# Kernel tuning notes

Hardware: AMD Instinct MI355X
Metric: run time of the kernel (lower is better)

The kernel has to match this reference:

```python
import jax, jax.numpy as jnp
import numpy as np

NO_EDGE_OFFSET_T_NORM = 2.0    # pushes no_edge above data range so min() ignores it
NO_EDGE_OFFSET_T_CONORM = -1.0 # pushes no_edge below data range so max() ignores it


def _daa_layer(x, sel, is_t_norm):
    """One DAALayer with a single operator for all nodes (LAYER_WISE init).

    x:   [B, in_features] float
    sel: [out_features, in_features] int, edge type per (node, input):
         0 = no_edge (value 0 + operator-dependent offset), 1 = normal_edge (value x)
    """
    off = NO_EDGE_OFFSET_T_NORM if is_t_norm else NO_EDGE_OFFSET_T_CONORM
    # [B, out, in]: gather edge values per node according to hard routing
    vals = jnp.where(sel[None, :, :] == 1, x[:, None, :], jnp.float32(off))
    # t-norm 'min' / t-conorm 'max' reduction over incoming edges
    return vals.min(axis=-1) if is_t_norm else vals.max(axis=-1)


def setup_inputs() -> dict:
    key = jax.random.key(0)
    k1, k2, k3 = jax.random.split(key, 3)
    B, IN, HID = 256, 1024, 512
    x = jax.random.uniform(k1, (B, IN), dtype=jnp.float32)
    # hard gumbel-softmax over all-ones logits == uniform edge-type choice
    sel0 = jax.random.randint(k2, (HID, IN), 0, 2)  # layer 0: 1024 -> 512
    sel1 = jax.random.randint(k3, (IN, HID), 0, 2)  # layer 1: 512 -> 1024
    return {"x": x, "sel0": sel0, "sel1": sel1}


def reference(x, sel0, sel1):
    h = _daa_layer(x, sel0, True)    # layer 0: T_Norm.min on all nodes
    out = _daa_layer(h, sel1, False)  # layer 1: T_Conorm.max on all nodes
    return out
```

## Files before the change

kernel.cpp:

```cpp
#include <hip/hip_runtime.h>
#include <hip/hip_fp16.h>


#define H_PINF 0x7C00u
#define H_NINF 0xFC00u

__device__ __forceinline__ unsigned pk_add(unsigned a, unsigned b) {
    unsigned r; asm("v_pk_add_f16 %0, %1, %2" : "=v"(r) : "v"(a), "v"(b)); return r;
}
__device__ __forceinline__ unsigned pk_min(unsigned a, unsigned b) {
    unsigned r; asm("v_pk_min_f16 %0, %1, %2" : "=v"(r) : "v"(a), "v"(b)); return r;
}
__device__ __forceinline__ unsigned pk_max(unsigned a, unsigned b) {
    unsigned r; asm("v_pk_max_f16 %0, %1, %2" : "=v"(r) : "v"(a), "v"(b)); return r;
}
__device__ __forceinline__ unsigned hpk(float a, float b) {
    return (unsigned)__half_as_ushort(__float2half(a))
         | ((unsigned)__half_as_ushort(__float2half(b)) << 16);
}
__device__ __forceinline__ float h2f(unsigned short u) {
    __half h = *reinterpret_cast<__half*>(&u);
    return __half2float(h);
}
__device__ __forceinline__ unsigned selpk(int a, int b, unsigned inf) {
    return (a ? 0u : inf) | ((b ? 0u : inf) << 16);
}

__global__ __launch_bounds__(1024) void daa_l0(
    const float* __restrict__ x, const int* __restrict__ sel0,
    uint4* __restrict__ hS)
{
    __shared__ unsigned aW[8 * 512];
    __shared__ uint4 xL[2][16 * 65];
    __shared__ unsigned red32[16 * 4 * 64];
    __shared__ unsigned mrg32[4 * 64];

    const int tid  = threadIdx.x;
    const int lane = tid & 63;
    const int s    = __builtin_amdgcn_readfirstlane(tid >> 6);
    const int bch  = blockIdx.x & 3;
    const int j    = blockIdx.x >> 2;
    const int b0   = bch * 64;

    {
        const int4* sp = (const int4*)sel0;
        const int row = tid >> 7, ch = tid & 127;
        const int4 v0 = sp[(size_t)(8 * j + row) * 256 + ch * 2 + 0];
        const int4 v1 = sp[(size_t)(8 * j + row) * 256 + ch * 2 + 1];
        unsigned* dst = &aW[row * 512 + ch * 4];
        dst[0] = selpk(v0.x, v0.y, H_PINF);
        dst[1] = selpk(v0.z, v0.w, H_PINF);
        dst[2] = selpk(v1.x, v1.y, H_PINF);
        dst[3] = selpk(v1.z, v1.w, H_PINF);
    }

    const int br = tid >> 4, cg = tid & 15;
#define STAGE(T, BUF)                                                      \
    do {                                                                   \
        const float* xr = x + (size_t)(b0 + br) * 1024 + (T) * 128 + cg * 8; \
        const float4 f0 = ((const float4*)xr)[0];                          \
        const float4 f1 = ((const float4*)xr)[1];                          \
        uint4 w;                                                           \
        w.x = hpk(f0.x, f0.y);  w.y = hpk(f0.z, f0.w);                     \
        w.z = hpk(f1.x, f1.y);  w.w = hpk(f1.z, f1.w);                     \
        xL[BUF][cg * 65 + br] = w;                                         \
    } while (0)

    STAGE(0, 0);
    __syncthreads();

    unsigned acc[8];
#pragma unroll
    for (int r = 0; r < 8; ++r) acc[r] = hpk(2.0f, 2.0f);

#pragma unroll
    for (int t = 0; t < 8; ++t) {
        if (t + 1 < 8) STAGE(t + 1, (t + 1) & 1);
        const uint4 xv = xL[t & 1][s * 65 + lane];
#pragma unroll
        for (int r = 0; r < 8; ++r) {
            const unsigned* a = &aW[r * 512 + t * 64 + s * 4];
            acc[r] = pk_min(acc[r], pk_add(xv.x, a[0]));
            acc[r] = pk_min(acc[r], pk_add(xv.y, a[1]));
            acc[r] = pk_min(acc[r], pk_add(xv.z, a[2]));
            acc[r] = pk_min(acc[r], pk_add(xv.w, a[3]));
        }
        __syncthreads();
    }
#undef STAGE

    {
#pragma unroll
        for (int u = 0; u < 4; ++u) {
            const unsigned flo = pk_min(acc[2 * u + 0], acc[2 * u + 0] >> 16);
            const unsigned fhi = pk_min(acc[2 * u + 1], acc[2 * u + 1] >> 16);
            red32[(s * 4 + u) * 64 + lane] = (flo & 0xffffu) | (fhi << 16);
        }
    }
    __syncthreads();

    if (tid < 256) {
        const int u = tid >> 6, ln = tid & 63;
        unsigned m = red32[u * 64 + ln];
#pragma unroll
        for (int ss = 1; ss < 16; ++ss)
            m = pk_min(m, red32[(ss * 4 + u) * 64 + ln]);
        mrg32[u * 64 + ln] = m;
    }
    __syncthreads();

    if (tid < 64) {
        uint4 w;
        w.x = mrg32[0 * 64 + tid];
        w.y = mrg32[1 * 64 + tid];
        w.z = mrg32[2 * 64 + tid];
        w.w = mrg32[3 * 64 + tid];
        hS[(size_t)bch * 4096 + (size_t)j * 64 + tid] = w;
    }
}

__global__ __launch_bounds__(1024) void daa_l1(
    const uint4* __restrict__ hS, const int* __restrict__ sel1,
    float* __restrict__ out)
{
    __shared__ unsigned aW[16 * 256];
    __shared__ unsigned red32[16 * 8 * 64];
    __shared__ float redf[16 * 65];

    const int tid  = threadIdx.x;
    const int lane = tid & 63;
    const int s    = __builtin_amdgcn_readfirstlane(tid >> 6);
    const int bch  = blockIdx.x & 3;
    const int j2   = blockIdx.x >> 2;
    const int b0   = bch * 64;

    {
        const int4* sp = (const int4*)sel1;
        const int row = tid >> 6, ch = tid & 63;
        const int4 v0 = sp[(size_t)(16 * j2 + row) * 128 + ch * 2 + 0];
        const int4 v1 = sp[(size_t)(16 * j2 + row) * 128 + ch * 2 + 1];
        unsigned* dst = &aW[row * 256 + ch * 4];
        dst[0] = selpk(v0.x, v0.y, H_NINF);
        dst[1] = selpk(v0.z, v0.w, H_NINF);
        dst[2] = selpk(v1.x, v1.y, H_NINF);
        dst[3] = selpk(v1.z, v1.w, H_NINF);
    }

    uint4 xh[4];
#pragma unroll
    for (int k = 0; k < 4; ++k)
        xh[k] = hS[(size_t)bch * 4096 + (size_t)(s * 4 + k) * 64 + lane];

    __syncthreads();

    unsigned acc[16];
#pragma unroll
    for (int r = 0; r < 16; ++r) acc[r] = hpk(-1.0f, -1.0f);

#pragma unroll
    for (int r = 0; r < 16; ++r) {
        const unsigned* a = &aW[r * 256 + s * 16];
#pragma unroll
        for (int k = 0; k < 4; ++k) {
            acc[r] = pk_max(acc[r], pk_add(xh[k].x, a[k * 4 + 0]));
            acc[r] = pk_max(acc[r], pk_add(xh[k].y, a[k * 4 + 1]));
            acc[r] = pk_max(acc[r], pk_add(xh[k].z, a[k * 4 + 2]));
            acc[r] = pk_max(acc[r], pk_add(xh[k].w, a[k * 4 + 3]));
        }
    }

    {
#pragma unroll
        for (int u = 0; u < 8; ++u) {
            const unsigned flo = pk_max(acc[2 * u + 0], acc[2 * u + 0] >> 16);
            const unsigned fhi = pk_max(acc[2 * u + 1], acc[2 * u + 1] >> 16);
            red32[(s * 8 + u) * 64 + lane] = (flo & 0xffffu) | (fhi << 16);
        }
    }
    __syncthreads();

    if (tid < 512) {
        const int u = tid >> 6, ln = tid & 63;
        unsigned m = red32[u * 64 + ln];
#pragma unroll
        for (int ss = 1; ss < 16; ++ss)
            m = pk_max(m, red32[(ss * 8 + u) * 64 + ln]);
        redf[(2 * u + 0) * 65 + ln] = h2f((unsigned short)(m & 0xffffu));
        redf[(2 * u + 1) * 65 + ln] = h2f((unsigned short)(m >> 16));
    }
    __syncthreads();

    {
        const int b = tid >> 4, ol = tid & 15;
        out[(size_t)(b0 + b) * 1024 + 16 * j2 + ol] = redf[ol * 65 + b];
    }
}

extern "C" void kernel_launch(void* const* d_in, const int* in_sizes, int n_in,
                              void* d_out, int out_size, void* d_ws, size_t ws_size,
                              hipStream_t stream) {
    const float* x    = (const float*)d_in[0];
    const int*   sel0 = (const int*)d_in[1];
    const int*   sel1 = (const int*)d_in[2];
    float* out = (float*)d_out;

    uint4* hS = (uint4*)d_ws;

    daa_l0<<<256, 1024, 0, stream>>>(x, sel0, hS);
    daa_l1<<<256, 1024, 0, stream>>>(hS, sel1, out);
}
```

Measured before the change: 21.45 us.

## Stage x in two large halves instead of eight tiles to cut barriers

Layer 0 now loads x into shared memory in two 512-column halves instead of eight 128-column tiles. This reduces the main loop from eight barriers to two and issues more global loads at once per thread. The reduction scratch arrays now alias the x staging buffer to offset the larger LDS footprint (about 133KB). The larger shared memory use may limit blocks per CU, and the second half's load is only overlapped with the first half's compute.

```diff
diff --git a/kernel.cpp b/kernel.cpp
--- a/kernel.cpp
+++ b/kernel.cpp
@@ -30,10 +30,8 @@
     const float* __restrict__ x, const int* __restrict__ sel0,
     uint4* __restrict__ hS)
 {
+    __shared__ uint4 xL[2][64 * 65];
     __shared__ unsigned aW[8 * 512];
-    __shared__ uint4 xL[2][16 * 65];
-    __shared__ unsigned red32[16 * 4 * 64];
-    __shared__ unsigned mrg32[4 * 64];
 
     const int tid  = threadIdx.x;
     const int lane = tid & 63;
@@ -54,40 +52,53 @@
         dst[3] = selpk(v1.z, v1.w, H_PINF);
     }
 
-    const int br = tid >> 4, cg = tid & 15;
-#define STAGE(T, BUF)                                                      \
+    const int br = tid >> 4, c = tid & 15;
+#define STAGE(H)                                                           \
     do {                                                                   \
-        const float* xr = x + (size_t)(b0 + br) * 1024 + (T) * 128 + cg * 8; \
-        const float4 f0 = ((const float4*)xr)[0];                          \
-        const float4 f1 = ((const float4*)xr)[1];                          \
-        uint4 w;                                                           \
-        w.x = hpk(f0.x, f0.y);  w.y = hpk(f0.z, f0.w);                     \
-        w.z = hpk(f1.x, f1.y);  w.w = hpk(f1.z, f1.w);                     \
-        xL[BUF][cg * 65 + br] = w;                                         \
+        const float* xr = x + (size_t)(b0 + br) * 1024 + (H) * 512;        \
+        _Pragma("unroll")                                                  \
+        for (int k = 0; k < 4; ++k) {                                      \
+            const int cg = c + k * 16;                                     \
+            const float4 f0 = ((const float4*)(xr + cg * 8))[0];           \
+            const float4 f1 = ((const float4*)(xr + cg * 8))[1];           \
+            uint4 w;                                                       \
+            w.x = hpk(f0.x, f0.y);  w.y = hpk(f0.z, f0.w);                 \
+            w.z = hpk(f1.x, f1.y);  w.w = hpk(f1.z, f1.w);                 \
+            xL[H][cg * 65 + br] = w;                                       \
+        }                                                                  \
     } while (0)
 
-    STAGE(0, 0);
-    __syncthreads();
+    STAGE(0);
+    __syncthreads();
+    STAGE(1);
 
     unsigned acc[8];
 #pragma unroll
     for (int r = 0; r < 8; ++r) acc[r] = hpk(2.0f, 2.0f);
 
-#pragma unroll
-    for (int t = 0; t < 8; ++t) {
-        if (t + 1 < 8) STAGE(t + 1, (t + 1) & 1);
-        const uint4 xv = xL[t & 1][s * 65 + lane];
-#pragma unroll
-        for (int r = 0; r < 8; ++r) {
-            const unsigned* a = &aW[r * 512 + t * 64 + s * 4];
-            acc[r] = pk_min(acc[r], pk_add(xv.x, a[0]));
-            acc[r] = pk_min(acc[r], pk_add(xv.y, a[1]));
-            acc[r] = pk_min(acc[r], pk_add(xv.z, a[2]));
-            acc[r] = pk_min(acc[r], pk_add(xv.w, a[3]));
-        }
-        __syncthreads();
-    }
+#define HALF(H)                                                            \
+    _Pragma("unroll")                                                      \
+    for (int t = 0; t < 4; ++t) {              \
+        const uint4 xv = xL[H][(t * 16 + s) * 65 + lane];                  \
+        _Pragma("unroll")                                                  \
+        for (int r = 0; r < 8; ++r) {                                      \
+            const unsigned* a = &aW[r * 512 + ((H) * 64 + t * 16 + s) * 4];\
+            acc[r] = pk_min(acc[r], pk_add(xv.x, a[0]));                   \
+            acc[r] = pk_min(acc[r], pk_add(xv.y, a[1]));                   \
+            acc[r] = pk_min(acc[r], pk_add(xv.z, a[2]));                   \
+            acc[r] = pk_min(acc[r], pk_add(xv.w, a[3]));                   \
+        }                                                                  \
+    }
+
+    HALF(0);
+    __syncthreads();
+    HALF(1);
+#undef HALF
 #undef STAGE
+
+    __syncthreads();
+    unsigned* red32 = (unsigned*)&xL[0][0];
+    unsigned* mrg32 = red32 + 16 * 4 * 64;
 
     {
 #pragma unroll
```

After: 23.07 us. 7.6% more time.
